# Kernel tuning notes

Measured on AMD Instinct MI355X. Metric: run time of the kernel, lower is better.

## Reference

```python
import jax, jax.numpy as jnp
import numpy as np

B, T, D, L, S = 128, 96, 800, 128, 10  # batch, time, features, latent, MC samples (hard-coded 10 in source)
LOG2PI = float(np.log(2.0 * np.pi))
RAW_SIGMA_BIAS = 0.5


def _linear_params(key, out_dim, in_dim):
    s = 1.0 / np.sqrt(in_dim)
    kw, kb = jax.random.split(key)
    W = jax.random.uniform(kw, (out_dim, in_dim), minval=-s, maxval=s, dtype=jnp.float32)
    b = jax.random.uniform(kb, (out_dim,), minval=-s, maxval=s, dtype=jnp.float32)
    return W, b


def setup_inputs() -> dict:
    key = jax.random.key(0)
    ks = jax.random.split(key, 12)
    W_px, b_px = _linear_params(ks[0], L, D)        # phi_x
    W_pz, b_pz = _linear_params(ks[1], L, L)        # phi_z
    W_pr, b_pr = _linear_params(ks[2], 2 * L, L)    # prior
    W_en, b_en = _linear_params(ks[3], 2 * L, 2 * L)  # encoder
    W_de, b_de = _linear_params(ks[4], D, 2 * L)    # decoder
    s = 1.0 / np.sqrt(L)
    W_ih = jax.random.uniform(ks[5], (4 * L, 2 * L), minval=-s, maxval=s, dtype=jnp.float32)
    W_hh = jax.random.uniform(ks[6], (4 * L, L), minval=-s, maxval=s, dtype=jnp.float32)
    b_ih = jax.random.uniform(ks[7], (4 * L,), minval=-s, maxval=s, dtype=jnp.float32)
    b_hh = jax.random.uniform(ks[8], (4 * L,), minval=-s, maxval=s, dtype=jnp.float32)
    inputs = jax.random.uniform(ks[9], (B, T, D), dtype=jnp.float32)  # four-hot-ish data in [0,1]
    eps = jax.random.normal(ks[10], (T, B, S, L), dtype=jnp.float32)  # reparameterization noise
    beta = jnp.ones((1,), jnp.float32)
    return dict(inputs=inputs, beta=beta, eps=eps, W_px=W_px, b_px=b_px, W_pz=W_pz, b_pz=b_pz,
                W_pr=W_pr, b_pr=b_pr, W_en=W_en, b_en=b_en, W_de=W_de, b_de=b_de,
                W_ih=W_ih, W_hh=W_hh, b_ih=b_ih, b_hh=b_hh)


def _vrnn_loss(inputs, beta, eps, W_px, b_px, W_pz, b_pz, W_pr, b_pr, W_en, b_en, W_de, b_de, W_ih, W_hh, b_ih, b_hh):
    Bsz, Tlen, _ = inputs.shape
    Lat = W_px.shape[0]
    mean_ = jnp.float32(0.0)  # self.mean logit offset
    b_lstm = b_ih + b_hh

    def lstm_step(carry, x_s):
        h, c = carry
        gates = x_s @ W_ih.T + h @ W_hh.T + b_lstm  # [B, 4L], torch gate order i,f,g,o
        i, f, g, o = jnp.split(gates, 4, axis=-1)
        c = jax.nn.sigmoid(f) * c + jax.nn.sigmoid(i) * jnp.tanh(g)
        h = jax.nn.sigmoid(o) * jnp.tanh(c)
        return (h, c), h

    def step(carry, xs):
        out, h, c = carry
        x, eps_t = xs  # [B,D], [B,S,L]
        x_hat = jax.nn.relu(x @ W_px.T + b_px)  # [B,L]
        # prior
        ph = jax.nn.relu(out @ W_pr.T + b_pr)
        mu_p, ls_p = jnp.split(ph, 2, axis=-1)
        sigma_p = jnp.maximum(jax.nn.softplus(jnp.exp(ls_p) + RAW_SIGMA_BIAS), 0.0)
        # posterior (mu shifted by prior mu)
        eh = jax.nn.relu(jnp.concatenate([out, x_hat], axis=-1) @ W_en.T + b_en)
        mu_q, ls_q = jnp.split(eh, 2, axis=-1)
        mu_q = mu_q + mu_p
        sigma_q = jnp.exp(ls_q)
        # 10-way reparameterized sampling
        z = mu_q[:, None, :] + sigma_q[:, None, :] * eps_t  # [B,S,L]
        z_hat = jax.nn.relu(z @ W_pz.T + b_pz)  # [B,S,L]
        out_b = jnp.broadcast_to(out[:, None, :], z_hat.shape)
        logits = jax.nn.relu(jnp.concatenate([z_hat, out_b], axis=-1) @ W_de.T + b_de) + mean_  # [B,S,D]
        # Bernoulli log-prob: x*l - softplus(l), summed over features
        log_px = jnp.sum(logits * x[:, None, :] - jax.nn.softplus(logits), axis=-1)  # [B,S]
        log_pz = jnp.sum(-0.5 * jnp.square((z - mu_p[:, None, :]) / sigma_p[:, None, :])
                         - jnp.log(sigma_p)[:, None, :] - 0.5 * LOG2PI, axis=-1)  # [B,S]
        log_qz = jnp.sum(-0.5 * jnp.square((z - mu_q[:, None, :]) / sigma_q[:, None, :])
                         - jnp.log(sigma_q)[:, None, :] - 0.5 * LOG2PI, axis=-1)  # [B,S]
        kl = log_qz - log_pz
        elbo = jnp.mean(log_px - beta * kl, axis=-1)  # [B], MC average over S samples
        # LSTM over the S samples as a length-S sequence (as in the source)
        rnn_in = jnp.concatenate([jnp.broadcast_to(x_hat[:, None, :], z_hat.shape), z_hat], axis=-1)  # [B,S,2L]
        (h, c), outs = jax.lax.scan(lstm_step, (h, c), jnp.swapaxes(rnn_in, 0, 1))  # outs [S,B,L]
        out_new = jnp.mean(outs, axis=0)  # [B,L] (mean over samples, matching h_out semantics)
        return (out_new, h, c), elbo

    zeros = jnp.zeros((Bsz, Lat), inputs.dtype)
    xs = (jnp.swapaxes(inputs, 0, 1), eps)  # time-major
    _, elbos = jax.lax.scan(step, (zeros, zeros, zeros), xs)  # [T,B]
    return -jnp.mean(jnp.sum(elbos, axis=0) / Tlen)


def reference(inputs, beta, eps, W_px, b_px, W_pz, b_pz, W_pr, b_pr, W_en, b_en, W_de, b_de, W_ih, W_hh, b_ih, b_hh):
    return _vrnn_loss(inputs, beta, eps, W_px, b_px, W_pz, b_pz, W_pr, b_pr,
                      W_en, b_en, W_de, b_de, W_ih, W_hh, b_ih, b_hh)
```

## Files before the change

### kernel.cpp

```cpp
#include <hip/hip_runtime.h>
#include <math.h>

#define TT 96
#define BB 128
#define DD 800
#define LL 128

typedef _Float16 h2v __attribute__((ext_vector_type(2)));
typedef _Float16 f16x8 __attribute__((ext_vector_type(8)));
typedef float f32x4 __attribute__((ext_vector_type(4)));

constexpr size_t O_WPX   = 0;
constexpr size_t O_WPR   = O_WPX   + 102400;
constexpr size_t O_WEN   = O_WPR   + 16384;
constexpr size_t O_BFENX = O_WEN   + 32768;
constexpr size_t O_BFIZ  = O_BFENX + 16384;
constexpr size_t O_BFHH  = O_BFIZ  + 32768;
constexpr size_t O_BFDE  = O_BFHH  + 32768;
constexpr size_t O_BFPZ  = O_BFDE  + 102400;
constexpr size_t O_BL    = O_BFPZ  + 8192;
constexpr size_t O_ACC   = O_BL    + 512;
constexpr size_t O_PROG  = O_ACC   + 4;
constexpr size_t O_XHAT  = O_PROG  + 128;
constexpr size_t O_GX    = O_XHAT  + 786432;
constexpr size_t O_ENCX  = O_GX    + 6291456;
constexpr size_t O_OUT   = O_ENCX  + 3145728;
constexpr size_t O_Q2    = O_OUT   + 1572864;
constexpr size_t O_P2    = O_Q2    + 3145728;

__device__ __forceinline__ h2v u2h(unsigned u) {
  union { unsigned u; h2v h; } x; x.u = u; return x.h;
}
__device__ __forceinline__ float fdot2(unsigned w, unsigned v, float acc) {
  return __builtin_amdgcn_fdot2(u2h(w), u2h(v), acc, false);
}
__device__ __forceinline__ unsigned packf16(float a, float b) {
  union { _Float16 h[2]; unsigned u; } x;
  x.h[0] = (_Float16)a; x.h[1] = (_Float16)b;
  return x.u;
}
__device__ __forceinline__ f16x8 u4h8(uint4 u) {
  union { uint4 u; f16x8 h; } x; x.u = u; return x.h;
}
__device__ __forceinline__ f32x4 mfma16(uint4 a, uint4 b, f32x4 c) {
  return __builtin_amdgcn_mfma_f32_16x16x32_f16(u4h8(a), u4h8(b), c, 0, 0, 0);
}
__device__ __forceinline__ float frcp(float x) { return __builtin_amdgcn_rcpf(x); }
__device__ __forceinline__ float fsigm(float x) { return frcp(1.f + __expf(-x)); }
__device__ __forceinline__ float ftanh(float x) {
  float e = __expf(2.f * fabsf(x));
  float t = 1.f - 2.f * frcp(e + 1.f);
  return copysignf(t, x);
}
__device__ __forceinline__ float hsum4(float4 a) { return (a.x + a.y) + (a.z + a.w); }

__device__ __forceinline__ void dotacc4(uint4 wv, uint4 vv, float4& av) {
  av.x = fdot2(wv.x, vv.x, av.x);
  av.y = fdot2(wv.y, vv.y, av.y);
  av.z = fdot2(wv.z, vv.z, av.z);
  av.w = fdot2(wv.w, vv.w, av.w);
}

__device__ __forceinline__ void bar_lds() {
  asm volatile("s_waitcnt lgkmcnt(0)" ::: "memory");
  __builtin_amdgcn_sched_barrier(0);
  __builtin_amdgcn_s_barrier();
  __builtin_amdgcn_sched_barrier(0);
}

__device__ __forceinline__ void gstore(float* p, float v) {
  __hip_atomic_store(p, v, __ATOMIC_RELAXED, __HIP_MEMORY_SCOPE_AGENT);
}
__device__ __forceinline__ float gload(const float* p) {
  return __hip_atomic_load(p, __ATOMIC_RELAXED, __HIP_MEMORY_SCOPE_AGENT);
}
__device__ __forceinline__ void gstore2(float2* p, float a, float b) {
  union { float f[2]; unsigned long long u; } x; x.f[0] = a; x.f[1] = b;
  __hip_atomic_store((unsigned long long*)p, x.u, __ATOMIC_RELAXED, __HIP_MEMORY_SCOPE_AGENT);
}
__device__ __forceinline__ float2 gload2(const float2* p) {
  unsigned long long u = __hip_atomic_load((const unsigned long long*)p,
                                           __ATOMIC_RELAXED, __HIP_MEMORY_SCOPE_AGENT);
  union { unsigned long long u; float2 f; } x; x.u = u; return x.f;
}

__device__ __forceinline__ int swz128(int row, int col) {
  return row * 128 + (col ^ ((row & 7) << 3));
}
__device__ __forceinline__ int swz256(int row, int col) {
  return row * 256 + (col ^ ((row & 7) << 3));
}

__device__ __forceinline__ void pack_f16_body(const float* __restrict__ src,
                                              unsigned* __restrict__ dst,
                                              int J, int rs, int k0, int idx, int total) {
  if (idx >= total) return;
  int u = idx & 3;
  int t2 = idx >> 2;
  int k8 = t2 / J;
  int j = t2 - k8 * J;
  int k = k8 * 8 + u * 2;
  const float* r = src + (size_t)j * rs + k0 + k;
  dst[idx] = packf16(r[0], r[1]);
}

__device__ __forceinline__ void bfrag_body(const float* __restrict__ src,
                                           unsigned* __restrict__ dst,
                                           int rs, int k0, int KS, int mode,
                                           int idx, int total) {
  if (idx >= total) return;
  int jj = idx & 3;
  int lane = (idx >> 2) & 63;
  int t2 = idx >> 8;
  int ks = t2 % KS;
  int g = t2 / KS;
  int n = (mode == 0) ? (128 * (g & 3) + 16 * (g >> 2) + (lane & 15))
                      : (16 * g + (lane & 15));
  int k = ks * 32 + (lane >> 4) * 8 + jj * 2;
  const float* r = src + (size_t)n * rs + k0 + k;
  dst[idx] = packf16(r[0], r[1]);
}

__device__ __forceinline__ void transpose_body(const float* __restrict__ src,
                                               float* __restrict__ dst,
                                               int J, int rs, int k0, int idx, int total) {
  if (idx >= total) return;
  int J4 = J * 4;
  int k4 = idx / J4;
  int rem = idx - k4 * J4;
  int j = rem >> 2;
  int kk = rem & 3;
  dst[idx] = src[j * rs + k0 + k4 * 4 + kk];
}

__global__ __launch_bounds__(256) void prep_all(
    const float* __restrict__ b_ih, const float* __restrict__ b_hh,
    const float* __restrict__ W_pr, const float* __restrict__ W_en,
    const float* __restrict__ W_ih, const float* __restrict__ W_hh,
    const float* __restrict__ W_pz, const float* __restrict__ W_de,
    const float* __restrict__ W_px, float* __restrict__ ws)
{
  int blk = blockIdx.x;
  const int tid = threadIdx.x;
  if (blk < 3) {
    if (blk < 2) {
      int i = blk * 256 + tid;
      ws[O_BL + i] = b_ih[i] + b_hh[i];
    } else {
      if (tid == 0) *(double*)(ws + O_ACC) = 0.0;
      if (tid < 128)
        __hip_atomic_store((int*)(ws + O_PROG) + tid, 0, __ATOMIC_RELAXED,
                           __HIP_MEMORY_SCOPE_AGENT);
    }
    return;
  }
  blk -= 3;
  if (blk < 64) { pack_f16_body(W_pr, (unsigned*)(ws + O_WPR), 256, 128, 0, blk * 256 + tid, 16384); return; }
  blk -= 64;
  if (blk < 64) { pack_f16_body(W_en, (unsigned*)(ws + O_WEN), 256, 256, 0, blk * 256 + tid, 16384); return; }
  blk -= 64;
  if (blk < 64) { bfrag_body(W_en, (unsigned*)(ws + O_BFENX), 256, 128, 4, 1, blk * 256 + tid, 16384); return; }
  blk -= 64;
  if (blk < 128) { bfrag_body(W_ih, (unsigned*)(ws + O_BFIZ), 256, 128, 4, 0, blk * 256 + tid, 32768); return; }
  blk -= 128;
  if (blk < 128) { bfrag_body(W_hh, (unsigned*)(ws + O_BFHH), 128, 0, 4, 0, blk * 256 + tid, 32768); return; }
  blk -= 128;
  if (blk < 32) { bfrag_body(W_pz, (unsigned*)(ws + O_BFPZ), 128, 0, 4, 1, blk * 256 + tid, 8192); return; }
  blk -= 32;
  if (blk < 400) { bfrag_body(W_de, (unsigned*)(ws + O_BFDE), 256, 0, 8, 1, blk * 256 + tid, 102400); return; }
  blk -= 400;
  transpose_body(W_px, ws + O_WPX, 128, 800, 0, blk * 256 + tid, 102400);
}

__device__ __forceinline__ float dot4(float4 w, float4 v) {
  return w.x*v.x + w.y*v.y + w.z*v.z + w.w*v.w;
}
__global__ __launch_bounds__(256) void xhat_kernel(const float* __restrict__ x,
                                                   const float* __restrict__ Wpx4,
                                                   const float* __restrict__ b_px,
                                                   unsigned* __restrict__ xhat2) {
  __shared__ __align__(16) float sx[16][800];
  const int wg = blockIdx.x, tid = threadIdx.x;
  const int p0 = wg * 16;
  for (int r = 0; r < 16; ++r) {
    int p = p0 + r; int t = p >> 7; int b = p & 127;
    const float* row = x + ((size_t)b * TT + t) * 800;
    for (int col = tid; col < 800; col += 256) sx[r][col] = row[col];
  }
  __syncthreads();
  const int j = tid & 127, g = tid >> 7;
  float acc[8];
  const float bj = b_px[j];
  #pragma unroll
  for (int u = 0; u < 8; ++u) acc[u] = bj;
  const float4* W = (const float4*)Wpx4;
  #pragma unroll 2
  for (int k4 = 0; k4 < 200; ++k4) {
    float4 w = W[k4 * 128 + j];
    #pragma unroll
    for (int u = 0; u < 8; ++u) {
      float4 xv = *(const float4*)&sx[g + 2*u][k4 * 4];
      acc[u] += dot4(w, xv);
    }
  }
  #pragma unroll
  for (int u = 0; u < 8; ++u) {
    float v = fmaxf(acc[u], 0.f);
    float vp = __shfl_xor(v, 1, 64);
    if ((j & 1) == 0) {
      int p = p0 + g + 2*u;
      xhat2[(size_t)p * 64 + (j >> 1)] = packf16(v, vp);
    }
  }
}

__global__ __launch_bounds__(512) void prep_gx(
    const unsigned* __restrict__ xhat2, const uint4* __restrict__ BFihz,
    const uint4* __restrict__ BFenx, const float* __restrict__ b_lstm,
    float* __restrict__ gxh, float* __restrict__ encx) {
  const int tid = threadIdx.x;
  const int wv = tid >> 6, lane = tid & 63, l15 = lane & 15, quad = lane >> 4;
  const int p0 = blockIdx.x * 16;
  uint4 a[4];
  #pragma unroll
  for (int ks = 0; ks < 4; ++ks)
    a[ks] = *(const uint4*)&xhat2[(size_t)(p0 + l15) * 64 + ks * 16 + quad * 4];
  #pragma unroll
  for (int nt = 0; nt < 4; ++nt) {
    int g = wv * 4 + nt;
    int n = 128 * (g & 3) + 16 * (g >> 2) + l15;
    float bl = b_lstm[n];
    f32x4 acc = {0.f, 0.f, 0.f, 0.f};
    #pragma unroll
    for (int ks = 0; ks < 4; ++ks)
      acc = mfma16(a[ks], BFihz[(g * 4 + ks) * 64 + lane], acc);
    #pragma unroll
    for (int r = 0; r < 4; ++r)
      gxh[(size_t)(p0 + quad * 4 + r) * 512 + n] = acc[r] + bl;
  }
  #pragma unroll
  for (int gt = 0; gt < 2; ++gt) {
    int g = wv * 2 + gt;
    f32x4 acc = {0.f, 0.f, 0.f, 0.f};
    #pragma unroll
    for (int ks = 0; ks < 4; ++ks)
      acc = mfma16(a[ks], BFenx[(g * 4 + ks) * 64 + lane], acc);
    #pragma unroll
    for (int r = 0; r < 4; ++r)
      encx[(size_t)(p0 + quad * 4 + r) * 256 + 16 * g + l15] = acc[r];
  }
}

__global__ __launch_bounds__(512) void fused_kernel(
    const float* __restrict__ eps,
    const uint4* __restrict__ Wpr4, const float* __restrict__ b_pr,
    const uint4* __restrict__ Wen4, const float* __restrict__ b_en,
    const uint4* __restrict__ BFpz, const float* __restrict__ b_pz,
    const uint4* __restrict__ BFihz, const uint4* __restrict__ BFhh,
    const float* __restrict__ gxh_g, const float* __restrict__ encx_g,
    float* __restrict__ g_out, float2* __restrict__ g_q2, float2* __restrict__ g_p2,
    const float* __restrict__ x, const float* __restrict__ beta_p,
    const uint4* __restrict__ BFde, const float* __restrict__ b_de,
    double* __restrict__ accum, int* __restrict__ prog)
{
  __shared__ __align__(16) char SMEM[161536];
  const int tid = threadIdx.x;

  if (blockIdx.x < 128) {
    float* s_gz       = (float*)SMEM;
    float* s_ehmu     = (float*)SMEM;
    float* s_mup      = (float*)(SMEM + 512);
    float* s_sgp      = (float*)(SMEM + 1024);
    float* s_sgq      = (float*)(SMEM + 1536);
    _Float16* s_z2    = (_Float16*)(SMEM + 20480);
    _Float16* s_zh2   = (_Float16*)(SMEM + 24832);
    float* s_out      = (float*)(SMEM + 29184);
    unsigned* s_out2  = (unsigned*)(SMEM + 29696);
    _Float16* s_h2    = (_Float16*)(SMEM + 29952);
    uint4* s_bfihz    = (uint4*)(SMEM + 30464);

    const int b = blockIdx.x;
    const int wv = tid >> 6;
    const int lane = tid & 63;
    const int l15 = lane & 15;
    const int quad = lane >> 4;

    #pragma unroll
    for (int i = 0; i < 16; ++i)
      s_bfihz[i * 512 + tid] = BFihz[i * 512 + tid];

    if (tid < 128) { s_out[tid] = 0.f; s_h2[tid] = (_Float16)0.f; }
    if (tid < 64) s_out2[tid] = 0u;
    float c_reg = 0.f;
    const float bias_pe = (tid < 256) ? b_pr[tid] : b_en[tid - 256];
    const float bz = b_pz[16 * wv + l15];
    const int gxoff = 16 * wv + l15;

    uint4 whhf[16], bfpz[4];
    #pragma unroll
    for (int i = 0; i < 16; ++i) whhf[i] = BFhh[(wv * 16 + i) * 64 + lane];
    #pragma unroll
    for (int ks = 0; ks < 4; ++ks) bfpz[ks] = BFpz[(wv * 4 + ks) * 64 + lane];

    float e0 = eps[(size_t)b * 1280 + tid];
    float e1 = eps[(size_t)b * 1280 + tid + 512];
    float e2 = (tid < 256) ? eps[(size_t)b * 1280 + tid + 1024] : 0.f;
    float gxf[4];
    #pragma unroll
    for (int nt = 0; nt < 4; ++nt)
      gxf[nt] = gxh_g[(size_t)b * 512 + 128 * nt + gxoff];
    float encx_r = (tid >= 256) ? encx_g[(size_t)b * 256 + (tid - 256)] : 0.f;

    __syncthreads();

    for (int t = 0; t < TT; ++t) {
      const size_t pb = (size_t)t * BB + b;

      {
        float4 a4 = {bias_pe, 0.f, 0.f, 0.f};
        if (tid < 256) {
          #pragma unroll 4
          for (int k8 = 0; k8 < 16; ++k8) {
            uint4 w = Wpr4[k8 * 256 + tid];
            uint4 o = *(const uint4*)&s_out2[k8 * 4];
            dotacc4(w, o, a4);
          }
          float ph = fmaxf(hsum4(a4), 0.f);
          if (tid < 128) s_mup[tid] = ph;
          else {
            float y = __expf(ph) + 0.5f;
            float sp = (y > 20.f) ? y : __logf(1.f + __expf(y));
            s_sgp[tid - 128] = sp;
          }
        } else {
          int j2 = tid - 256;
          #pragma unroll 4
          for (int k8 = 0; k8 < 16; ++k8) {
            uint4 w = Wen4[k8 * 256 + j2];
            uint4 o = *(const uint4*)&s_out2[k8 * 4];
            dotacc4(w, o, a4);
          }
          float eh = fmaxf(hsum4(a4) + encx_r, 0.f);
          if (j2 < 128) s_ehmu[j2] = eh;
          else s_sgq[j2 - 128] = __expf(eh);
        }
      }
      bar_lds();

      {
        int l = tid & 127, s0 = tid >> 7;
        float mu = s_ehmu[l] + s_mup[l];
        float sq = s_sgq[l];
        s_z2[s0 * 136 + l]        = (_Float16)(mu + sq * e0);
        s_z2[(s0 + 4) * 136 + l]  = (_Float16)(mu + sq * e1);
        if (tid < 256) s_z2[(s0 + 8) * 136 + l] = (_Float16)(mu + sq * e2);
      }
      bar_lds();

      if (tid < 128) {
        gstore2(&g_q2[pb * 128 + tid], s_ehmu[tid] + s_mup[tid], s_sgq[tid]);
      } else if (tid < 256) {
        gstore(&g_out[pb * 128 + tid - 128], s_out[tid - 128]);
      } else if (tid < 384) {
        int l = tid - 256;
        gstore2(&g_p2[pb * 128 + l], s_mup[l], s_sgp[l]);
      }

      {
        uint4 a[4];
        #pragma unroll
        for (int ks = 0; ks < 4; ++ks)
          a[ks] = *(const uint4*)&s_z2[l15 * 136 + ks * 32 + quad * 8];
        f32x4 acc = {bz, bz, bz, bz};
        #pragma unroll
        for (int ks = 0; ks < 4; ++ks)
          acc = mfma16(a[ks], bfpz[ks], acc);
        #pragma unroll
        for (int r = 0; r < 4; ++r) {
          int s = quad * 4 + r;
          if (s < 10)
            s_zh2[s * 136 + 16 * wv + l15] = (_Float16)fmaxf(acc[r], 0.f);
        }
      }
      bar_lds();

      {
        uint4 a[4];
        #pragma unroll
        for (int ks = 0; ks < 4; ++ks)
          a[ks] = *(const uint4*)&s_zh2[l15 * 136 + ks * 32 + quad * 8];
        #pragma unroll
        for (int nt = 0; nt < 4; ++nt) {
          float gx = gxf[nt];
          f32x4 acc = {gx, gx, gx, gx};
          #pragma unroll
          for (int ks = 0; ks < 4; ++ks)
            acc = mfma16(a[ks], s_bfihz[((wv * 4 + nt) * 4 + ks) * 64 + lane], acc);
          #pragma unroll
          for (int r = 0; r < 4; ++r) {
            int s = quad * 4 + r;
            if (s < 10)
              s_gz[s * 512 + 128 * nt + 16 * wv + l15] = acc[r];
          }
        }
      }
      __syncthreads();

      if (tid == 0)
        __hip_atomic_store(&prog[b], t + 1, __ATOMIC_RELAXED, __HIP_MEMORY_SCOPE_AGENT);

      if (t + 1 < TT) {
        const float* epn = eps + (pb + BB) * 1280;
        e0 = epn[tid];
        e1 = epn[tid + 512];
        if (tid < 256) e2 = epn[tid + 1024];
        #pragma unroll
        for (int nt = 0; nt < 4; ++nt)
          gxf[nt] = gxh_g[(pb + BB) * 512 + 128 * nt + gxoff];
        if (tid >= 256) encx_r = encx_g[(pb + BB) * 256 + (tid - 256)];
      }

      float oacc = 0.f;
      for (int s = 0; s < 10; ++s) {
        const _Float16* hb = &s_h2[(s & 1) * 128];
        uint4 a[4];
        #pragma unroll
        for (int ks = 0; ks < 4; ++ks)
          a[ks] = *(const uint4*)&hb[ks * 32 + quad * 8];
        f32x4 acc[4];
        #pragma unroll
        for (int nt = 0; nt < 4; ++nt) {
          float cz = s_gz[s * 512 + 128 * nt + 16 * wv + l15];
          acc[nt] = f32x4{cz, cz, cz, cz};
        }
        #pragma unroll
        for (int nt = 0; nt < 4; ++nt)
          #pragma unroll
          for (int ks = 0; ks < 4; ++ks)
            acc[nt] = mfma16(a[ks], whhf[nt * 4 + ks], acc[nt]);
        if (lane < 16) {
          float gi = acc[0][0], gf = acc[1][0], gg = acc[2][0], go = acc[3][0];
          c_reg = fsigm(gf) * c_reg + fsigm(gi) * ftanh(gg);
          float h = fsigm(go) * ftanh(c_reg);
          oacc += h;
          s_h2[((s + 1) & 1) * 128 + 16 * wv + lane] = (_Float16)h;
        }
        if (s < 9) bar_lds();
      }
      if (lane < 16) {
        float v = oacc * 0.1f;
        s_out[16 * wv + lane] = v;
        float vn = __shfl_xor(v, 1, 64);
        if (!(lane & 1)) s_out2[8 * wv + (lane >> 1)] = packf16(v, vn);
      }
      bar_lds();
    }
  } else {
    _Float16* c_z2   = (_Float16*)SMEM;
    _Float16* c_a2   = (_Float16*)(SMEM + 12288);
    float* c_x       = (float*)(SMEM + 36864);
    unsigned* c_out2 = (unsigned*)(SMEM + 49664);
    float* c_muq     = (float*)(SMEM + 50688);
    float* c_sgq     = (float*)(SMEM + 52736);
    float* c_mup     = (float*)(SMEM + 54784);
    float* c_sgp     = (float*)(SMEM + 56832);
    float* c_wred    = (float*)(SMEM + 58880);

    const int cid = blockIdx.x - 128;
    const int wv = tid >> 6;
    const int lane = tid & 63;
    const int l15 = lane & 15;
    const int quad = lane >> 4;
    const float beta = beta_p[0];

    for (int c = cid; c < 3072; c += 128) {
      const int p0 = c * 4;
      const int t = p0 >> 7;
      const int b0 = p0 & 127;

      if (tid < 4) {
        while (__hip_atomic_load(&prog[b0 + tid], __ATOMIC_RELAXED,
                                 __HIP_MEMORY_SCOPE_AGENT) <= t)
          __builtin_amdgcn_s_sleep(8);
      }
      __syncthreads();

      float acc_loc = 0.f;
      {
        size_t gi = (size_t)p0 * 128 + tid;
        float2 q = gload2(&g_q2[gi]); c_muq[tid] = q.x; c_sgq[tid] = q.y;
        float2 pv = gload2(&g_p2[gi]); c_mup[tid] = pv.x; c_sgp[tid] = pv.y;
      }
      if (tid < 256) {
        int pair = tid >> 6, m = tid & 63;
        const float* o = g_out + (size_t)p0 * 128 + pair * 128;
        c_out2[tid] = packf16(gload(o + 2*m), gload(o + 2*m + 1));
      }
      for (int i = tid; i < 3200; i += 512) {
        int pp = i / 800;
        int d = i - pp * 800;
        int p = p0 + pp, bb = p & 127, tt2 = p >> 7;
        c_x[i] = x[((size_t)bb * TT + tt2) * 800 + d];
      }
      __syncthreads();

      {
        int l = tid & 127, pp = tid >> 7;
        float mq = c_muq[pp*128 + l], sq = c_sgq[pp*128 + l];
        float mp = c_mup[pp*128 + l], spv = c_sgp[pp*128 + l];
        float inv_sp = frcp(spv);
        float lsq = __logf(sq), lsp = __logf(spv);
        const float* ep = eps + (size_t)(p0 + pp) * 1280 + l;
        float kl = 0.f;
        #pragma unroll
        for (int s = 0; s < 10; ++s) {
          float e = ep[s * 128];
          float z = mq + sq * e;
          c_z2[swz128(pp * 10 + s, l)] = (_Float16)z;
          float ap = (z - mp) * inv_sp;
          kl += (-0.5f * e * e - lsq) - (-0.5f * ap * ap - lsp);
        }
        acc_loc -= beta * kl;
      }
      for (int i = tid; i < 2560; i += 512) {
        int r = i >> 6, m = i & 63;
        int pp = (r * 205) >> 11;
        ((unsigned*)c_a2)[r * 128 + 64 + (m ^ ((r & 7) << 2))] = c_out2[pp * 64 + m];
      }
      __syncthreads();

      for (int tile = wv; tile < 24; tile += 8) {
        int mt = tile >> 3, nt = tile & 7;
        uint4 a[4];
        #pragma unroll
        for (int ks = 0; ks < 4; ++ks)
          a[ks] = *(const uint4*)&c_z2[swz128(mt * 16 + l15, ks * 32 + quad * 8)];
        float bzt = b_pz[16 * nt + l15];
        f32x4 acc = {bzt, bzt, bzt, bzt};
        #pragma unroll
        for (int ks = 0; ks < 4; ++ks)
          acc = mfma16(a[ks], BFpz[(nt * 4 + ks) * 64 + lane], acc);
        #pragma unroll
        for (int r = 0; r < 4; ++r) {
          int row = mt * 16 + quad * 4 + r;
          c_a2[swz256(row, 16 * nt + l15)] = (_Float16)fmaxf(acc[r], 0.f);
        }
      }
      __syncthreads();

      #pragma unroll
      for (int mt = 0; mt < 3; ++mt) {
        uint4 a[8];
        #pragma unroll
        for (int ks = 0; ks < 8; ++ks)
          a[ks] = *(const uint4*)&c_a2[swz256(mt * 16 + l15, ks * 32 + quad * 8)];
        for (int nt = wv; nt < 50; nt += 8) {
          f32x4 acc = {0.f, 0.f, 0.f, 0.f};
          #pragma unroll
          for (int ks = 0; ks < 8; ++ks)
            acc = mfma16(a[ks], BFde[(nt * 8 + ks) * 64 + lane], acc);
          int d = 16 * nt + l15;
          float bd = b_de[d];
          #pragma unroll
          for (int r = 0; r < 4; ++r) {
            int row = mt * 16 + quad * 4 + r;
            if (row < 40) {
              int pp = (row * 205) >> 11;
              float lg = fmaxf(acc[r] + bd, 0.f);
              float xd = c_x[pp * 800 + d];
              acc_loc += xd * lg - lg - __logf(1.f + __expf(-lg));
            }
          }
        }
      }

      float v = acc_loc;
      #pragma unroll
      for (int off = 32; off > 0; off >>= 1) v += __shfl_down(v, off, 64);
      if ((tid & 63) == 0) c_wred[tid >> 6] = v;
      __syncthreads();
      if (tid == 0) {
        double tot = 0.0;
        #pragma unroll
        for (int w = 0; w < 8; ++w) tot += (double)c_wred[w];
        atomicAdd(accum, tot);
      }
      __syncthreads();
    }
  }
}

__global__ void finalize_kernel(const double* __restrict__ accum, float* __restrict__ out) {
  if (threadIdx.x == 0 && blockIdx.x == 0)
    out[0] = (float)(-accum[0] / 122880.0);
}

extern "C" void kernel_launch(void* const* d_in, const int* in_sizes, int n_in,
                              void* d_out, int out_size, void* d_ws, size_t ws_size,
                              hipStream_t stream) {
  const float* x    = (const float*)d_in[0];
  const float* beta = (const float*)d_in[1];
  const float* eps  = (const float*)d_in[2];
  const float* W_px = (const float*)d_in[3];
  const float* b_px = (const float*)d_in[4];
  const float* W_pz = (const float*)d_in[5];
  const float* b_pz = (const float*)d_in[6];
  const float* W_pr = (const float*)d_in[7];
  const float* b_pr = (const float*)d_in[8];
  const float* W_en = (const float*)d_in[9];
  const float* b_en = (const float*)d_in[10];
  const float* W_de = (const float*)d_in[11];
  const float* b_de = (const float*)d_in[12];
  const float* W_ih = (const float*)d_in[13];
  const float* W_hh = (const float*)d_in[14];
  const float* b_ih = (const float*)d_in[15];
  const float* b_hh = (const float*)d_in[16];
  float* ws = (float*)d_ws;

  prep_all<<<dim3(1283), dim3(256), 0, stream>>>(
      b_ih, b_hh, W_pr, W_en, W_ih, W_hh, W_pz, W_de, W_px, ws);

  xhat_kernel<<<dim3(768), dim3(256), 0, stream>>>(
      x, ws + O_WPX, b_px, (unsigned*)(ws + O_XHAT));

  prep_gx<<<dim3(768), dim3(512), 0, stream>>>(
      (const unsigned*)(ws + O_XHAT), (const uint4*)(ws + O_BFIZ),
      (const uint4*)(ws + O_BFENX), ws + O_BL, ws + O_GX, ws + O_ENCX);

  {
    const uint4* Wpr4  = (const uint4*)(ws + O_WPR);
    const uint4* Wen4  = (const uint4*)(ws + O_WEN);
    const uint4* BFpz  = (const uint4*)(ws + O_BFPZ);
    const uint4* BFihz = (const uint4*)(ws + O_BFIZ);
    const uint4* BFhh  = (const uint4*)(ws + O_BFHH);
    const uint4* BFde  = (const uint4*)(ws + O_BFDE);
    const float* gxh   = ws + O_GX;
    const float* encx  = ws + O_ENCX;
    float* g_out = ws + O_OUT;
    float2* g_q2 = (float2*)(ws + O_Q2);
    float2* g_p2 = (float2*)(ws + O_P2);
    double* accum = (double*)(ws + O_ACC);
    int* prog = (int*)(ws + O_PROG);

    void* kargs[] = {
      (void*)&eps,
      (void*)&Wpr4, (void*)&b_pr, (void*)&Wen4, (void*)&b_en,
      (void*)&BFpz, (void*)&b_pz, (void*)&BFihz, (void*)&BFhh,
      (void*)&gxh, (void*)&encx,
      (void*)&g_out, (void*)&g_q2, (void*)&g_p2,
      (void*)&x, (void*)&beta,
      (void*)&BFde, (void*)&b_de,
      (void*)&accum, (void*)&prog
    };
    hipLaunchCooperativeKernel((void*)fused_kernel, dim3(256), dim3(512),
                               kargs, 0, stream);
  }

  finalize_kernel<<<dim3(1), dim3(64), 0, stream>>>((const double*)(ws + O_ACC), (float*)d_out);
}
```

Before: 994.9 us.

## Merge prep, xhat, gx and finalize kernels into one cooperative megakernel

Folds the weight-prep kernel, the phi_x projection, the input-gate/encoder precompute and the finalize step into a single cooperative kernel, with grid.sync barriers between phases. The xhat result now goes through shared memory instead of a global buffer, and x is read straight from global memory rather than staged in LDS. This removes four kernel launches and the xhat round trip. In exchange the prep phases run on only 256 blocks, the xhat GEMM loses its LDS reuse of x, and the kernel adds three grid-wide barriers.

```diff
diff --git a/kernel.cpp b/kernel.cpp
--- a/kernel.cpp
+++ b/kernel.cpp
@@ -1,5 +1,8 @@
 #include <hip/hip_runtime.h>
+#include <hip/hip_cooperative_groups.h>
 #include <math.h>
+
+namespace cg = cooperative_groups;
 
 #define TT 96
 #define BB 128
@@ -93,8 +96,7 @@
 
 __device__ __forceinline__ void pack_f16_body(const float* __restrict__ src,
                                               unsigned* __restrict__ dst,
-                                              int J, int rs, int k0, int idx, int total) {
-  if (idx >= total) return;
+                                              int J, int rs, int k0, int idx) {
   int u = idx & 3;
   int t2 = idx >> 2;
   int k8 = t2 / J;
@@ -106,9 +108,7 @@
 
 __device__ __forceinline__ void bfrag_body(const float* __restrict__ src,
                                            unsigned* __restrict__ dst,
-                                           int rs, int k0, int KS, int mode,
-                                           int idx, int total) {
-  if (idx >= total) return;
+                                           int rs, int k0, int KS, int mode, int idx) {
   int jj = idx & 3;
   int lane = (idx >> 2) & 63;
   int t2 = idx >> 8;
@@ -123,8 +123,7 @@
 
 __device__ __forceinline__ void transpose_body(const float* __restrict__ src,
                                                float* __restrict__ dst,
-                                               int J, int rs, int k0, int idx, int total) {
-  if (idx >= total) return;
+                                               int J, int rs, int k0, int idx) {
   int J4 = J * 4;
   int k4 = idx / J4;
   int rem = idx - k4 * J4;
@@ -133,140 +132,133 @@
   dst[idx] = src[j * rs + k0 + k4 * 4 + kk];
 }
 
-__global__ __launch_bounds__(256) void prep_all(
-    const float* __restrict__ b_ih, const float* __restrict__ b_hh,
-    const float* __restrict__ W_pr, const float* __restrict__ W_en,
-    const float* __restrict__ W_ih, const float* __restrict__ W_hh,
-    const float* __restrict__ W_pz, const float* __restrict__ W_de,
-    const float* __restrict__ W_px, float* __restrict__ ws)
-{
-  int blk = blockIdx.x;
-  const int tid = threadIdx.x;
-  if (blk < 3) {
-    if (blk < 2) {
-      int i = blk * 256 + tid;
-      ws[O_BL + i] = b_ih[i] + b_hh[i];
-    } else {
-      if (tid == 0) *(double*)(ws + O_ACC) = 0.0;
-      if (tid < 128)
-        __hip_atomic_store((int*)(ws + O_PROG) + tid, 0, __ATOMIC_RELAXED,
-                           __HIP_MEMORY_SCOPE_AGENT);
-    }
-    return;
-  }
-  blk -= 3;
-  if (blk < 64) { pack_f16_body(W_pr, (unsigned*)(ws + O_WPR), 256, 128, 0, blk * 256 + tid, 16384); return; }
-  blk -= 64;
-  if (blk < 64) { pack_f16_body(W_en, (unsigned*)(ws + O_WEN), 256, 256, 0, blk * 256 + tid, 16384); return; }
-  blk -= 64;
-  if (blk < 64) { bfrag_body(W_en, (unsigned*)(ws + O_BFENX), 256, 128, 4, 1, blk * 256 + tid, 16384); return; }
-  blk -= 64;
-  if (blk < 128) { bfrag_body(W_ih, (unsigned*)(ws + O_BFIZ), 256, 128, 4, 0, blk * 256 + tid, 32768); return; }
-  blk -= 128;
-  if (blk < 128) { bfrag_body(W_hh, (unsigned*)(ws + O_BFHH), 128, 0, 4, 0, blk * 256 + tid, 32768); return; }
-  blk -= 128;
-  if (blk < 32) { bfrag_body(W_pz, (unsigned*)(ws + O_BFPZ), 128, 0, 4, 1, blk * 256 + tid, 8192); return; }
-  blk -= 32;
-  if (blk < 400) { bfrag_body(W_de, (unsigned*)(ws + O_BFDE), 256, 0, 8, 1, blk * 256 + tid, 102400); return; }
-  blk -= 400;
-  transpose_body(W_px, ws + O_WPX, 128, 800, 0, blk * 256 + tid, 102400);
-}
-
 __device__ __forceinline__ float dot4(float4 w, float4 v) {
   return w.x*v.x + w.y*v.y + w.z*v.z + w.w*v.w;
 }
-__global__ __launch_bounds__(256) void xhat_kernel(const float* __restrict__ x,
-                                                   const float* __restrict__ Wpx4,
-                                                   const float* __restrict__ b_px,
-                                                   unsigned* __restrict__ xhat2) {
-  __shared__ __align__(16) float sx[16][800];
-  const int wg = blockIdx.x, tid = threadIdx.x;
-  const int p0 = wg * 16;
-  for (int r = 0; r < 16; ++r) {
-    int p = p0 + r; int t = p >> 7; int b = p & 127;
-    const float* row = x + ((size_t)b * TT + t) * 800;
-    for (int col = tid; col < 800; col += 256) sx[r][col] = row[col];
-  }
-  __syncthreads();
-  const int j = tid & 127, g = tid >> 7;
-  float acc[8];
-  const float bj = b_px[j];
-  #pragma unroll
-  for (int u = 0; u < 8; ++u) acc[u] = bj;
-  const float4* W = (const float4*)Wpx4;
-  #pragma unroll 2
-  for (int k4 = 0; k4 < 200; ++k4) {
-    float4 w = W[k4 * 128 + j];
-    #pragma unroll
-    for (int u = 0; u < 8; ++u) {
-      float4 xv = *(const float4*)&sx[g + 2*u][k4 * 4];
-      acc[u] += dot4(w, xv);
-    }
-  }
-  #pragma unroll
-  for (int u = 0; u < 8; ++u) {
-    float v = fmaxf(acc[u], 0.f);
-    float vp = __shfl_xor(v, 1, 64);
-    if ((j & 1) == 0) {
-      int p = p0 + g + 2*u;
-      xhat2[(size_t)p * 64 + (j >> 1)] = packf16(v, vp);
-    }
-  }
-}
-
-__global__ __launch_bounds__(512) void prep_gx(
-    const unsigned* __restrict__ xhat2, const uint4* __restrict__ BFihz,
-    const uint4* __restrict__ BFenx, const float* __restrict__ b_lstm,
-    float* __restrict__ gxh, float* __restrict__ encx) {
-  const int tid = threadIdx.x;
-  const int wv = tid >> 6, lane = tid & 63, l15 = lane & 15, quad = lane >> 4;
-  const int p0 = blockIdx.x * 16;
-  uint4 a[4];
-  #pragma unroll
-  for (int ks = 0; ks < 4; ++ks)
-    a[ks] = *(const uint4*)&xhat2[(size_t)(p0 + l15) * 64 + ks * 16 + quad * 4];
-  #pragma unroll
-  for (int nt = 0; nt < 4; ++nt) {
-    int g = wv * 4 + nt;
-    int n = 128 * (g & 3) + 16 * (g >> 2) + l15;
-    float bl = b_lstm[n];
-    f32x4 acc = {0.f, 0.f, 0.f, 0.f};
-    #pragma unroll
-    for (int ks = 0; ks < 4; ++ks)
-      acc = mfma16(a[ks], BFihz[(g * 4 + ks) * 64 + lane], acc);
-    #pragma unroll
-    for (int r = 0; r < 4; ++r)
-      gxh[(size_t)(p0 + quad * 4 + r) * 512 + n] = acc[r] + bl;
-  }
-  #pragma unroll
-  for (int gt = 0; gt < 2; ++gt) {
-    int g = wv * 2 + gt;
-    f32x4 acc = {0.f, 0.f, 0.f, 0.f};
-    #pragma unroll
-    for (int ks = 0; ks < 4; ++ks)
-      acc = mfma16(a[ks], BFenx[(g * 4 + ks) * 64 + lane], acc);
-    #pragma unroll
-    for (int r = 0; r < 4; ++r)
-      encx[(size_t)(p0 + quad * 4 + r) * 256 + 16 * g + l15] = acc[r];
-  }
-}
-
-__global__ __launch_bounds__(512) void fused_kernel(
+
+__global__ __launch_bounds__(512) void mega_kernel(
+    const float* __restrict__ x, const float* __restrict__ beta_p,
     const float* __restrict__ eps,
-    const uint4* __restrict__ Wpr4, const float* __restrict__ b_pr,
-    const uint4* __restrict__ Wen4, const float* __restrict__ b_en,
-    const uint4* __restrict__ BFpz, const float* __restrict__ b_pz,
-    const uint4* __restrict__ BFihz, const uint4* __restrict__ BFhh,
-    const float* __restrict__ gxh_g, const float* __restrict__ encx_g,
-    float* __restrict__ g_out, float2* __restrict__ g_q2, float2* __restrict__ g_p2,
-    const float* __restrict__ x, const float* __restrict__ beta_p,
-    const uint4* __restrict__ BFde, const float* __restrict__ b_de,
-    double* __restrict__ accum, int* __restrict__ prog)
+    const float* __restrict__ W_px, const float* __restrict__ b_px,
+    const float* __restrict__ W_pz, const float* __restrict__ b_pz,
+    const float* __restrict__ W_pr, const float* __restrict__ b_pr,
+    const float* __restrict__ W_en, const float* __restrict__ b_en,
+    const float* __restrict__ W_de, const float* __restrict__ b_de,
+    const float* __restrict__ W_ih, const float* __restrict__ W_hh,
+    const float* __restrict__ b_ih, const float* __restrict__ b_hh,
+    float* __restrict__ ws, float* __restrict__ out)
 {
   __shared__ __align__(16) char SMEM[161536];
   const int tid = threadIdx.x;
-
-  if (blockIdx.x < 128) {
+  const int bid = blockIdx.x;
+  cg::grid_group grid = cg::this_grid();
+
+  const uint4* Wpr4  = (const uint4*)(ws + O_WPR);
+  const uint4* Wen4  = (const uint4*)(ws + O_WEN);
+  const uint4* BFpz  = (const uint4*)(ws + O_BFPZ);
+  const uint4* BFihz = (const uint4*)(ws + O_BFIZ);
+  const uint4* BFhh  = (const uint4*)(ws + O_BFHH);
+  const uint4* BFde  = (const uint4*)(ws + O_BFDE);
+  const float* gxh_g  = ws + O_GX;
+  const float* encx_g = ws + O_ENCX;
+  float* g_out = ws + O_OUT;
+  float2* g_q2 = (float2*)(ws + O_Q2);
+  float2* g_p2 = (float2*)(ws + O_P2);
+  double* accum = (double*)(ws + O_ACC);
+  int* prog = (int*)(ws + O_PROG);
+
+  if (bid == 0) {
+    if (tid == 0) *accum = 0.0;
+    if (tid < 128)
+      __hip_atomic_store(&prog[tid], 0, __ATOMIC_RELAXED, __HIP_MEMORY_SCOPE_AGENT);
+  }
+  for (int it = bid * 512 + tid; it < 328192; it += 131072) {
+    if (it < 512)         ws[O_BL + it] = b_ih[it] + b_hh[it];
+    else if (it < 16896)  pack_f16_body(W_pr, (unsigned*)(ws + O_WPR), 256, 128, 0, it - 512);
+    else if (it < 33280)  pack_f16_body(W_en, (unsigned*)(ws + O_WEN), 256, 256, 0, it - 16896);
+    else if (it < 49664)  bfrag_body(W_en, (unsigned*)(ws + O_BFENX), 256, 128, 4, 1, it - 33280);
+    else if (it < 82432)  bfrag_body(W_ih, (unsigned*)(ws + O_BFIZ), 256, 128, 4, 0, it - 49664);
+    else if (it < 115200) bfrag_body(W_hh, (unsigned*)(ws + O_BFHH), 128, 0, 4, 0, it - 82432);
+    else if (it < 123392) bfrag_body(W_pz, (unsigned*)(ws + O_BFPZ), 128, 0, 4, 1, it - 115200);
+    else if (it < 225792) bfrag_body(W_de, (unsigned*)(ws + O_BFDE), 256, 0, 8, 1, it - 123392);
+    else                  transpose_body(W_px, ws + O_WPX, 128, 800, 0, it - 225792);
+  }
+  __threadfence();
+  grid.sync();
+
+  {
+    unsigned* s_xh = (unsigned*)SMEM;
+    const float4* W = (const float4*)(ws + O_WPX);
+    const int j = tid & 127, g = tid >> 7;
+    const int wv = tid >> 6, lane = tid & 63, l15 = lane & 15, quad = lane >> 4;
+    const float bj = b_px[j];
+
+    for (int i = 0; i < 3; ++i) {
+      const int tx = bid + 256 * i;
+      const int p0 = tx * 16;
+      int offs[4];
+      #pragma unroll
+      for (int u = 0; u < 4; ++u) {
+        int p = p0 + g + 4 * u;
+        int b_ = p & 127, t_ = p >> 7;
+        offs[u] = __builtin_amdgcn_readfirstlane((b_ * TT + t_) * 800);
+      }
+      float acc[4];
+      #pragma unroll
+      for (int u = 0; u < 4; ++u) acc[u] = bj;
+      #pragma unroll 2
+      for (int k4 = 0; k4 < 200; ++k4) {
+        float4 w = W[k4 * 128 + j];
+        #pragma unroll
+        for (int u = 0; u < 4; ++u) {
+          float4 xv = *(const float4*)(x + offs[u] + k4 * 4);
+          acc[u] += dot4(w, xv);
+        }
+      }
+      #pragma unroll
+      for (int u = 0; u < 4; ++u) {
+        float v = fmaxf(acc[u], 0.f);
+        float vp = __shfl_xor(v, 1, 64);
+        if ((j & 1) == 0)
+          s_xh[(g + 4 * u) * 68 + (j >> 1)] = packf16(v, vp);
+      }
+      __syncthreads();
+
+      uint4 a[4];
+      #pragma unroll
+      for (int ks = 0; ks < 4; ++ks)
+        a[ks] = *(const uint4*)&s_xh[l15 * 68 + ks * 16 + quad * 4];
+      #pragma unroll
+      for (int nt = 0; nt < 4; ++nt) {
+        int gg = wv * 4 + nt;
+        int n = 128 * (gg & 3) + 16 * (gg >> 2) + l15;
+        float bl = ws[O_BL + n];
+        f32x4 acc2 = {0.f, 0.f, 0.f, 0.f};
+        #pragma unroll
+        for (int ks = 0; ks < 4; ++ks)
+          acc2 = mfma16(a[ks], BFihz[(gg * 4 + ks) * 64 + lane], acc2);
+        #pragma unroll
+        for (int r = 0; r < 4; ++r)
+          ws[O_GX + (size_t)(p0 + quad * 4 + r) * 512 + n] = acc2[r] + bl;
+      }
+      #pragma unroll
+      for (int gt = 0; gt < 2; ++gt) {
+        int gg = wv * 2 + gt;
+        f32x4 acc2 = {0.f, 0.f, 0.f, 0.f};
+        #pragma unroll
+        for (int ks = 0; ks < 4; ++ks)
+          acc2 = mfma16(a[ks], ((const uint4*)(ws + O_BFENX))[(gg * 4 + ks) * 64 + lane], acc2);
+        #pragma unroll
+        for (int r = 0; r < 4; ++r)
+          ws[O_ENCX + (size_t)(p0 + quad * 4 + r) * 256 + 16 * gg + l15] = acc2[r];
+      }
+      __syncthreads();
+    }
+  }
+  __threadfence();
+  grid.sync();
+
+  if (bid < 128) {
     float* s_gz       = (float*)SMEM;
     float* s_ehmu     = (float*)SMEM;
     float* s_mup      = (float*)(SMEM + 512);
@@ -279,7 +271,7 @@
     _Float16* s_h2    = (_Float16*)(SMEM + 29952);
     uint4* s_bfihz    = (uint4*)(SMEM + 30464);
 
-    const int b = blockIdx.x;
+    const int b = bid;
     const int wv = tid >> 6;
     const int lane = tid & 63;
     const int l15 = lane & 15;
@@ -466,7 +458,7 @@
     float* c_sgp     = (float*)(SMEM + 56832);
     float* c_wred    = (float*)(SMEM + 58880);
 
-    const int cid = blockIdx.x - 128;
+    const int cid = bid - 128;
     const int wv = tid >> 6;
     const int lane = tid & 63;
     const int l15 = lane & 15;
@@ -588,11 +580,13 @@
       __syncthreads();
     }
   }
-}
-
-__global__ void finalize_kernel(const double* __restrict__ accum, float* __restrict__ out) {
-  if (threadIdx.x == 0 && blockIdx.x == 0)
-    out[0] = (float)(-accum[0] / 122880.0);
+
+  __threadfence();
+  grid.sync();
+  if (bid == 0 && tid == 0) {
+    double a = *(volatile double*)accum;
+    out[0] = (float)(-a / 122880.0);
+  }
 }
 
 extern "C" void kernel_launch(void* const* d_in, const int* in_sizes, int n_in,
@@ -616,45 +610,19 @@
   const float* b_ih = (const float*)d_in[15];
   const float* b_hh = (const float*)d_in[16];
   float* ws = (float*)d_ws;
-
-  prep_all<<<dim3(1283), dim3(256), 0, stream>>>(
-      b_ih, b_hh, W_pr, W_en, W_ih, W_hh, W_pz, W_de, W_px, ws);
-
-  xhat_kernel<<<dim3(768), dim3(256), 0, stream>>>(
-      x, ws + O_WPX, b_px, (unsigned*)(ws + O_XHAT));
-
-  prep_gx<<<dim3(768), dim3(512), 0, stream>>>(
-      (const unsigned*)(ws + O_XHAT), (const uint4*)(ws + O_BFIZ),
-      (const uint4*)(ws + O_BFENX), ws + O_BL, ws + O_GX, ws + O_ENCX);
-
-  {
-    const uint4* Wpr4  = (const uint4*)(ws + O_WPR);
-    const uint4* Wen4  = (const uint4*)(ws + O_WEN);
-    const uint4* BFpz  = (const uint4*)(ws + O_BFPZ);
-    const uint4* BFihz = (const uint4*)(ws + O_BFIZ);
-    const uint4* BFhh  = (const uint4*)(ws + O_BFHH);
-    const uint4* BFde  = (const uint4*)(ws + O_BFDE);
-    const float* gxh   = ws + O_GX;
-    const float* encx  = ws + O_ENCX;
-    float* g_out = ws + O_OUT;
-    float2* g_q2 = (float2*)(ws + O_Q2);
-    float2* g_p2 = (float2*)(ws + O_P2);
-    double* accum = (double*)(ws + O_ACC);
-    int* prog = (int*)(ws + O_PROG);
-
-    void* kargs[] = {
-      (void*)&eps,
-      (void*)&Wpr4, (void*)&b_pr, (void*)&Wen4, (void*)&b_en,
-      (void*)&BFpz, (void*)&b_pz, (void*)&BFihz, (void*)&BFhh,
-      (void*)&gxh, (void*)&encx,
-      (void*)&g_out, (void*)&g_q2, (void*)&g_p2,
-      (void*)&x, (void*)&beta,
-      (void*)&BFde, (void*)&b_de,
-      (void*)&accum, (void*)&prog
-    };
-    hipLaunchCooperativeKernel((void*)fused_kernel, dim3(256), dim3(512),
-                               kargs, 0, stream);
-  }
-
-  finalize_kernel<<<dim3(1), dim3(64), 0, stream>>>((const double*)(ws + O_ACC), (float*)d_out);
-}
+  float* out = (float*)d_out;
+
+  void* kargs[] = {
+    (void*)&x, (void*)&beta, (void*)&eps,
+    (void*)&W_px, (void*)&b_px,
+    (void*)&W_pz, (void*)&b_pz,
+    (void*)&W_pr, (void*)&b_pr,
+    (void*)&W_en, (void*)&b_en,
+    (void*)&W_de, (void*)&b_de,
+    (void*)&W_ih, (void*)&W_hh,
+    (void*)&b_ih, (void*)&b_hh,
+    (void*)&ws, (void*)&out
+  };
+  hipLaunchCooperativeKernel((void*)mega_kernel, dim3(256), dim3(512),
+                             kargs, 0, stream);
+}
```

New measurement: 1.258 ms. 1.26x slower.

## Fuse phi_x projection and LSTM/encoder input GEMMs into one kernel

Applied to the files above, without the earlier changes.

Merges the xhat kernel and the prep_gx kernel into one launch, so the relu'd fp16 phi_x rows stay in shared memory instead of going through global memory. It also drops the shared-memory staging of the input rows: each thread reads x directly from global with wave-uniform offsets, and the block now uses 512 threads covering 16 rows at 4 rows per thread. This removes one launch and the xhat global round-trip. The cost is uncached global reads of x inside the k loop in place of LDS reuse.

```diff
diff --git a/kernel.cpp b/kernel.cpp
--- a/kernel.cpp
+++ b/kernel.cpp
@@ -175,79 +175,77 @@
 __device__ __forceinline__ float dot4(float4 w, float4 v) {
   return w.x*v.x + w.y*v.y + w.z*v.z + w.w*v.w;
 }
-__global__ __launch_bounds__(256) void xhat_kernel(const float* __restrict__ x,
-                                                   const float* __restrict__ Wpx4,
-                                                   const float* __restrict__ b_px,
-                                                   unsigned* __restrict__ xhat2) {
-  __shared__ __align__(16) float sx[16][800];
-  const int wg = blockIdx.x, tid = threadIdx.x;
-  const int p0 = wg * 16;
-  for (int r = 0; r < 16; ++r) {
-    int p = p0 + r; int t = p >> 7; int b = p & 127;
-    const float* row = x + ((size_t)b * TT + t) * 800;
-    for (int col = tid; col < 800; col += 256) sx[r][col] = row[col];
-  }
-  __syncthreads();
+
+__global__ __launch_bounds__(512) void xhat_gx_kernel(
+    const float* __restrict__ x, const float* __restrict__ Wpx4,
+    const float* __restrict__ b_px,
+    const uint4* __restrict__ BFihz, const uint4* __restrict__ BFenx,
+    const float* __restrict__ b_lstm,
+    float* __restrict__ gxh, float* __restrict__ encx)
+{
+  __shared__ __align__(16) unsigned s_xh[16 * 68];
+  const int tid = threadIdx.x;
   const int j = tid & 127, g = tid >> 7;
-  float acc[8];
+  const int wv = tid >> 6, lane = tid & 63, l15 = lane & 15, quad = lane >> 4;
+  const int p0 = blockIdx.x * 16;
+
+  int offs[4];
+  #pragma unroll
+  for (int u = 0; u < 4; ++u) {
+    int p = p0 + g + 4 * u;
+    int b_ = p & 127, t_ = p >> 7;
+    offs[u] = __builtin_amdgcn_readfirstlane((b_ * TT + t_) * 800);
+  }
   const float bj = b_px[j];
+  float acc[4];
   #pragma unroll
-  for (int u = 0; u < 8; ++u) acc[u] = bj;
+  for (int u = 0; u < 4; ++u) acc[u] = bj;
   const float4* W = (const float4*)Wpx4;
   #pragma unroll 2
   for (int k4 = 0; k4 < 200; ++k4) {
     float4 w = W[k4 * 128 + j];
     #pragma unroll
-    for (int u = 0; u < 8; ++u) {
-      float4 xv = *(const float4*)&sx[g + 2*u][k4 * 4];
+    for (int u = 0; u < 4; ++u) {
+      float4 xv = *(const float4*)(x + offs[u] + k4 * 4);
       acc[u] += dot4(w, xv);
     }
   }
   #pragma unroll
-  for (int u = 0; u < 8; ++u) {
+  for (int u = 0; u < 4; ++u) {
     float v = fmaxf(acc[u], 0.f);
     float vp = __shfl_xor(v, 1, 64);
-    if ((j & 1) == 0) {
-      int p = p0 + g + 2*u;
-      xhat2[(size_t)p * 64 + (j >> 1)] = packf16(v, vp);
-    }
-  }
-}
-
-__global__ __launch_bounds__(512) void prep_gx(
-    const unsigned* __restrict__ xhat2, const uint4* __restrict__ BFihz,
-    const uint4* __restrict__ BFenx, const float* __restrict__ b_lstm,
-    float* __restrict__ gxh, float* __restrict__ encx) {
-  const int tid = threadIdx.x;
-  const int wv = tid >> 6, lane = tid & 63, l15 = lane & 15, quad = lane >> 4;
-  const int p0 = blockIdx.x * 16;
+    if ((j & 1) == 0)
+      s_xh[(g + 4 * u) * 68 + (j >> 1)] = packf16(v, vp);
+  }
+  __syncthreads();
+
   uint4 a[4];
   #pragma unroll
   for (int ks = 0; ks < 4; ++ks)
-    a[ks] = *(const uint4*)&xhat2[(size_t)(p0 + l15) * 64 + ks * 16 + quad * 4];
+    a[ks] = *(const uint4*)&s_xh[l15 * 68 + ks * 16 + quad * 4];
   #pragma unroll
   for (int nt = 0; nt < 4; ++nt) {
-    int g = wv * 4 + nt;
-    int n = 128 * (g & 3) + 16 * (g >> 2) + l15;
+    int gg = wv * 4 + nt;
+    int n = 128 * (gg & 3) + 16 * (gg >> 2) + l15;
     float bl = b_lstm[n];
-    f32x4 acc = {0.f, 0.f, 0.f, 0.f};
+    f32x4 acc2 = {0.f, 0.f, 0.f, 0.f};
     #pragma unroll
     for (int ks = 0; ks < 4; ++ks)
-      acc = mfma16(a[ks], BFihz[(g * 4 + ks) * 64 + lane], acc);
+      acc2 = mfma16(a[ks], BFihz[(gg * 4 + ks) * 64 + lane], acc2);
     #pragma unroll
     for (int r = 0; r < 4; ++r)
-      gxh[(size_t)(p0 + quad * 4 + r) * 512 + n] = acc[r] + bl;
+      gxh[(size_t)(p0 + quad * 4 + r) * 512 + n] = acc2[r] + bl;
   }
   #pragma unroll
   for (int gt = 0; gt < 2; ++gt) {
-    int g = wv * 2 + gt;
-    f32x4 acc = {0.f, 0.f, 0.f, 0.f};
+    int gg = wv * 2 + gt;
+    f32x4 acc2 = {0.f, 0.f, 0.f, 0.f};
     #pragma unroll
     for (int ks = 0; ks < 4; ++ks)
-      acc = mfma16(a[ks], BFenx[(g * 4 + ks) * 64 + lane], acc);
+      acc2 = mfma16(a[ks], BFenx[(gg * 4 + ks) * 64 + lane], acc2);
     #pragma unroll
     for (int r = 0; r < 4; ++r)
-      encx[(size_t)(p0 + quad * 4 + r) * 256 + 16 * g + l15] = acc[r];
+      encx[(size_t)(p0 + quad * 4 + r) * 256 + 16 * gg + l15] = acc2[r];
   }
 }
 
@@ -620,12 +618,10 @@
   prep_all<<<dim3(1283), dim3(256), 0, stream>>>(
       b_ih, b_hh, W_pr, W_en, W_ih, W_hh, W_pz, W_de, W_px, ws);
 
-  xhat_kernel<<<dim3(768), dim3(256), 0, stream>>>(
-      x, ws + O_WPX, b_px, (unsigned*)(ws + O_XHAT));
-
-  prep_gx<<<dim3(768), dim3(512), 0, stream>>>(
-      (const unsigned*)(ws + O_XHAT), (const uint4*)(ws + O_BFIZ),
-      (const uint4*)(ws + O_BFENX), ws + O_BL, ws + O_GX, ws + O_ENCX);
+  xhat_gx_kernel<<<dim3(768), dim3(512), 0, stream>>>(
+      x, ws + O_WPX, b_px,
+      (const uint4*)(ws + O_BFIZ), (const uint4*)(ws + O_BFENX),
+      ws + O_BL, ws + O_GX, ws + O_ENCX);
 
   {
     const uint4* Wpr4  = (const uint4*)(ws + O_WPR);
```

Result: faster. 967.6 us (-2.7%).
